# Optimization experiments

Hardware: AMD Instinct MI355X
Metric: run time of the kernel (lower is better)

## Reference

```python
import jax, jax.numpy as jnp
import numpy as np

# DCRNN (PEMS-BAY scale) constants
N = 325      # num_nodes
B = 64       # batch_size
T = 12       # encoder seq_len
HZ = 12      # decoder horizon
U = 64       # rnn_units
DIN = 2      # input_dim
DOUT = 1     # output_dim
K = 2        # max_diffusion_step
NM = K + 1   # num diffusion matrices (Chebyshev, single laplacian support)


def _glorot(key, shape):
    lim = float(np.sqrt(6.0 / (shape[0] + shape[1])))
    return jax.random.uniform(key, shape, jnp.float32, -lim, lim)


def setup_inputs() -> dict:
    key = jax.random.key(0)
    ks = jax.random.split(key, 8)
    # random symmetric adjacency -> scaled Laplacian support (lambda_max ~= 2 approx)
    a = np.asarray(jax.random.uniform(ks[0], (N, N)))
    a = (a + a.T) * 0.5
    a = a * (a > 0.9)
    d = a.sum(1)
    dinv = 1.0 / np.sqrt(np.maximum(d, 1e-8))
    L = np.eye(N, dtype=np.float32) - (dinv[:, None] * a * dinv[None, :]).astype(np.float32)
    support = jnp.asarray(L - np.eye(N, dtype=np.float32))  # 2L/lambda_max - I with lambda_max=2

    def cell_params(k, din):
        f = (din + U) * NM
        k1, k2 = jax.random.split(k)
        return dict(gate_W=_glorot(k1, (f, 2 * U)), gate_b=jnp.zeros((2 * U,), jnp.float32),
                    cand_W=_glorot(k2, (f, U)), cand_b=jnp.zeros((U,), jnp.float32))

    inp = {"inputs": jax.random.normal(ks[1], (T, B, N * DIN), jnp.float32),
           "support": support}
    for name, din, kk in [("enc0", DIN, ks[2]), ("enc1", U, ks[3]),
                          ("dec0", DOUT, ks[4]), ("dec1", U, ks[5])]:
        for pn, v in cell_params(kk, din).items():
            inp[f"{name}_{pn}"] = v
    inp["proj_W"] = _glorot(ks[6], (U, DOUT))
    inp["proj_b"] = jnp.zeros((DOUT,), jnp.float32)
    return inp


def _gconv(x, support, W, b):
    # x: (B, N, F). Chebyshev diffusion: x0=x, x1=Lx, x2=2Lx1-x0, ...
    xs = [x]
    x0, x1 = x, jnp.einsum('mn,bnf->bmf', support, x)
    xs.append(x1)
    for _ in range(2, K + 1):
        x2 = 2.0 * jnp.einsum('mn,bnf->bmf', support, x1) - x0
        xs.append(x2)
        x0, x1 = x1, x2
    xk = jnp.concatenate(xs, axis=-1)  # (B, N, NM*F)
    return xk @ W + b


def _gru_cell(x, h, support, gW, gb, cW, cb):
    # diffusion-conv GRU: r,u gates then candidate
    ru = jax.nn.sigmoid(_gconv(jnp.concatenate([x, h], -1), support, gW, gb))
    r, u = jnp.split(ru, 2, axis=-1)
    c = jnp.tanh(_gconv(jnp.concatenate([x, r * h], -1), support, cW, cb))
    return u * h + (1.0 - u) * c


def reference(inputs, support,
              enc0_gate_W, enc0_gate_b, enc0_cand_W, enc0_cand_b,
              enc1_gate_W, enc1_gate_b, enc1_cand_W, enc1_cand_b,
              dec0_gate_W, dec0_gate_b, dec0_cand_W, dec0_cand_b,
              dec1_gate_W, dec1_gate_b, dec1_cand_W, dec1_cand_b,
              proj_W, proj_b):
    x_seq = inputs.reshape(T, B, N, DIN)
    h0 = jnp.zeros((B, N, U), inputs.dtype)

    def enc_step(carry, x):
        h_l0, h_l1 = carry
        h_l0 = _gru_cell(x, h_l0, support, enc0_gate_W, enc0_gate_b, enc0_cand_W, enc0_cand_b)
        h_l1 = _gru_cell(h_l0, h_l1, support, enc1_gate_W, enc1_gate_b, enc1_cand_W, enc1_cand_b)
        return (h_l0, h_l1), None

    (h_l0, h_l1), _ = jax.lax.scan(enc_step, (h0, h0), x_seq)

    def dec_step(carry, _):
        d_in, hd0, hd1 = carry
        hd0 = _gru_cell(d_in, hd0, support, dec0_gate_W, dec0_gate_b, dec0_cand_W, dec0_cand_b)
        hd1 = _gru_cell(hd0, hd1, support, dec1_gate_W, dec1_gate_b, dec1_cand_W, dec1_cand_b)
        out = hd1 @ proj_W + proj_b  # (B, N, DOUT)
        return (out, hd0, hd1), out.reshape(B, N * DOUT)

    start = jnp.zeros((B, N, DOUT), inputs.dtype)  # GO symbol
    _, outputs = jax.lax.scan(dec_step, (start, h_l0, h_l1), None, length=HZ)
    return outputs  # (horizon, B, N*DOUT)
```

## Files before the change

kernel.cpp:

```cpp
#include <hip/hip_runtime.h>

constexpr int N  = 325;
constexpr int B  = 64;
constexpr int T  = 12;
constexpr int HZ = 12;
constexpr int U  = 64;
constexpr int BN = B * N;

constexpr int SSTIL = 42;
constexpr int SSKC  = 11;
constexpr int XST   = 364;

typedef __attribute__((ext_vector_type(8))) short short8;
typedef __attribute__((ext_vector_type(4))) float floatx4;

__device__ inline unsigned short f2bf(float f) {
    unsigned u = __float_as_uint(f);
    u += 0x7fff + ((u >> 16) & 1);
    return (unsigned short)(u >> 16);
}
__device__ inline unsigned pack_hilo(float v) {
    const unsigned short hi = f2bf(v);
    const float hif = __uint_as_float(((unsigned)hi) << 16);
    const unsigned short lo = f2bf(v - hif);
    return (unsigned)hi | ((unsigned)lo << 16);
}
__device__ inline void unpack8(const uint4 u0, const uint4 u1,
                               short8& h, short8& l) {
    const unsigned uu[8] = {u0.x, u0.y, u0.z, u0.w, u1.x, u1.y, u1.z, u1.w};
    #pragma unroll
    for (int j = 0; j < 8; ++j) {
        h[j] = (short)(uu[j] & 0xffffu);
        l[j] = (short)(uu[j] >> 16);
    }
}


__global__ void zero_kernel(unsigned* __restrict__ p, long n) {
    long i = (long)blockIdx.x * blockDim.x + threadIdx.x;
    const long stride = (long)gridDim.x * blockDim.x;
    for (; i < n; i += stride) p[i] = 0u;
}

__global__ __launch_bounds__(256)
void s2_build(const float* __restrict__ S, float* __restrict__ S2)
{
    const int m = blockIdx.x;
    __shared__ float srow[N];
    for (int i = threadIdx.x; i < N; i += 256) srow[i] = S[m * N + i];
    __syncthreads();
    for (int c = threadIdx.x; c < N; c += 256) {
        float a = 0.f;
        for (int k = 0; k < N; ++k) a += srow[k] * S[k * N + c];
        S2[m * N + c] = a;
    }
}

__global__ __launch_bounds__(64)
void prepack_ss(const float* __restrict__ S, const float* __restrict__ S2,
                short* __restrict__ ssh, short* __restrict__ ssl)
{
    const int t = blockIdx.x, kc = blockIdx.y, lane = threadIdx.x;
    const int quad = lane >> 4, l15 = lane & 15;
    short8 hv, lv;
    #pragma unroll
    for (int j = 0; j < 8; ++j) {
        const int m = t * 16 + l15;
        const int k = kc * 32 + quad * 8 + j;
        float v = 0.f;
        if (k < N) {
            if (m < N) v = S[m * N + k];
            else if (m >= 336 && m < 336 + N) v = S2[(m - 336) * N + k];
        }
        const unsigned short hb = f2bf(v);
        hv[j] = (short)hb;
        lv[j] = (short)f2bf(v - __uint_as_float(((unsigned)hb) << 16));
    }
    const size_t off = ((size_t)(t * SSKC + kc) * 64 + lane);
    ((short8*)ssh)[off] = hv;
    ((short8*)ssl)[off] = lv;
}

__global__ __launch_bounds__(64)
void prepack_w(const float* __restrict__ W, short* __restrict__ Wh,
               short* __restrict__ Wl, int F, int Nout, int NT, int Z0KC)
{
    const int kc = blockIdx.x, n = blockIdx.y, lane = threadIdx.x;
    const int quad = lane >> 4, l15 = lane & 15;
    short8 hv, lv;
    #pragma unroll
    for (int j = 0; j < 8; ++j) {
        const int p   = kc * 32 + quad * 8 + j;
        const int col = n * 16 + l15;
        float w = 0.f;
        if (p < Z0KC * 32) {
            const int f = p;
            if (f < F)
                w = W[(size_t)f * Nout + col] - W[(size_t)(2 * F + f) * Nout + col];
        } else {
            const int q = p - Z0KC * 32;
            if (q < F)
                w = W[(size_t)(F + q) * Nout + col];
            else if (q < 2 * F)
                w = 2.f * W[(size_t)(2 * F + (q - F)) * Nout + col];
        }
        const unsigned short hb = f2bf(w);
        hv[j] = (short)hb;
        lv[j] = (short)f2bf(w - __uint_as_float(((unsigned)hb) << 16));
    }
    const size_t off = ((size_t)(kc * NT + n) * 64 + lane);
    ((short8*)Wh)[off] = hv;
    ((short8*)Wl)[off] = lv;
}

template<int DIN, int F, bool RM, bool ZV>
__device__ __forceinline__ void z0_frag(const float* __restrict__ x,
    const float* __restrict__ h, const float* __restrict__ ru,
    int row, int kc, int quad, short8& ah, short8& al)
{
    float v[8];
    if constexpr (ZV) {
        const int k0 = kc * 32 + quad * 8;
        if (k0 < 64) {
            const float4 a = *(const float4*)&x[(size_t)row * 64 + k0];
            const float4 b = *(const float4*)&x[(size_t)row * 64 + k0 + 4];
            v[0]=a.x; v[1]=a.y; v[2]=a.z; v[3]=a.w;
            v[4]=b.x; v[5]=b.y; v[6]=b.z; v[7]=b.w;
        } else {
            const int kk = k0 - 64;
            float4 a = *(const float4*)&h[(size_t)row * 64 + kk];
            float4 b = *(const float4*)&h[(size_t)row * 64 + kk + 4];
            if constexpr (RM) {
                const float4 ra = *(const float4*)&ru[(size_t)row * 128 + kk];
                const float4 rb = *(const float4*)&ru[(size_t)row * 128 + kk + 4];
                a.x *= ra.x; a.y *= ra.y; a.z *= ra.z; a.w *= ra.w;
                b.x *= rb.x; b.y *= rb.y; b.z *= rb.z; b.w *= rb.w;
            }
            v[0]=a.x; v[1]=a.y; v[2]=a.z; v[3]=a.w;
            v[4]=b.x; v[5]=b.y; v[6]=b.z; v[7]=b.w;
        }
    } else {
        #pragma unroll
        for (int j = 0; j < 8; ++j) {
            const int k = kc * 32 + quad * 8 + j;
            float t = 0.f;
            if (k < DIN) t = x[(size_t)row * DIN + k];
            else if (k < F) {
                t = h[(size_t)row * 64 + (k - DIN)];
                if constexpr (RM) t *= ru[(size_t)row * 128 + (k - DIN)];
            }
            v[j] = t;
        }
    }
    #pragma unroll
    for (int j = 0; j < 8; ++j) {
        const unsigned u = pack_hilo(v[j]);
        ah[j] = (short)(u & 0xffffu);
        al[j] = (short)(u >> 16);
    }
}

template<int DIN, int F, int YP, bool RMUL, bool VEC>
__device__ __forceinline__ void diffuse_body(
    const short8* __restrict__ ssh, const short8* __restrict__ ssl,
    const float* __restrict__ x, const float* __restrict__ h,
    const float* __restrict__ ru, unsigned* __restrict__ zcat,
    int cx, int b, unsigned* __restrict__ xls)
{
    const int c0 = cx * 32;
    const int tid = threadIdx.x, wave = tid >> 6, lane = tid & 63;
    const int quad = lane >> 4, l15 = lane & 15;

    if constexpr (VEC) {
        for (int idx4 = tid; idx4 < 352 * 8; idx4 += 896) {
            const int n = idx4 >> 3, f = (idx4 & 7) * 4, gf = c0 + f;
            uint4 pk = make_uint4(0u, 0u, 0u, 0u);
            if (n < N) {
                const int row = b * N + n;
                float4 v;
                if (gf < DIN) {
                    v = *(const float4*)&x[(size_t)row * DIN + gf];
                } else {
                    v = *(const float4*)&h[(size_t)row * U + (gf - DIN)];
                    if (RMUL) {
                        const float4 rv = *(const float4*)&ru[(size_t)row * 128 + (gf - DIN)];
                        v.x *= rv.x; v.y *= rv.y; v.z *= rv.z; v.w *= rv.w;
                    }
                }
                pk.x = pack_hilo(v.x); pk.y = pack_hilo(v.y);
                pk.z = pack_hilo(v.z); pk.w = pack_hilo(v.w);
            }
            xls[(f + 0) * XST + n] = pk.x;
            xls[(f + 1) * XST + n] = pk.y;
            xls[(f + 2) * XST + n] = pk.z;
            xls[(f + 3) * XST + n] = pk.w;
        }
    } else {
        for (int idx = tid; idx < 352 * 32; idx += 896) {
            const int n = idx >> 5, f = idx & 31, gf = c0 + f;
            unsigned u = 0u;
            if (n < N && gf < F) {
                const int row = b * N + n;
                float v;
                if (gf < DIN) {
                    v = x[(size_t)row * DIN + gf];
                } else {
                    v = h[(size_t)row * U + (gf - DIN)];
                    if (RMUL) v *= ru[(size_t)row * 128 + (gf - DIN)];
                }
                u = pack_hilo(v);
            }
            xls[f * XST + n] = u;
        }
    }
    __syncthreads();

    const int tb = wave * 3;

    floatx4 acc[3][2];
    #pragma unroll
    for (int i = 0; i < 3; ++i)
        #pragma unroll
        for (int n = 0; n < 2; ++n)
            acc[i][n] = (floatx4){0.f, 0.f, 0.f, 0.f};

    short8 cah[3], cal[3], nah[3], nal[3];
    #pragma unroll
    for (int i = 0; i < 3; ++i) {
        const size_t fo = (size_t)((tb + i) * SSKC) * 64 + lane;
        cah[i] = ssh[fo]; cal[i] = ssl[fo];
    }
    for (int kc = 0; kc < SSKC; ++kc) {
        if (kc + 1 < SSKC) {
            #pragma unroll
            for (int i = 0; i < 3; ++i) {
                const size_t fo = (size_t)((tb + i) * SSKC + kc + 1) * 64 + lane;
                nah[i] = ssh[fo]; nal[i] = ssl[fo];
            }
        }
        short8 bh[2], bl[2];
        const int koff = kc * 32 + quad * 8;
        #pragma unroll
        for (int n = 0; n < 2; ++n) {
            const uint4 u0 = *(const uint4*)&xls[(n * 16 + l15) * XST + koff];
            const uint4 u1 = *(const uint4*)&xls[(n * 16 + l15) * XST + koff + 4];
            unpack8(u0, u1, bh[n], bl[n]);
        }
        #pragma unroll
        for (int i = 0; i < 3; ++i)
            #pragma unroll
            for (int n = 0; n < 2; ++n) {
                acc[i][n] = __builtin_amdgcn_mfma_f32_16x16x32_bf16(cah[i], bh[n], acc[i][n], 0, 0, 0);
                acc[i][n] = __builtin_amdgcn_mfma_f32_16x16x32_bf16(cah[i], bl[n], acc[i][n], 0, 0, 0);
                acc[i][n] = __builtin_amdgcn_mfma_f32_16x16x32_bf16(cal[i], bh[n], acc[i][n], 0, 0, 0);
            }
        if (kc + 1 < SSKC) {
            #pragma unroll
            for (int i = 0; i < 3; ++i) { cah[i] = nah[i]; cal[i] = nal[i]; }
        }
    }

    #pragma unroll
    for (int i = 0; i < 3; ++i) {
        const int t = tb + i;
        #pragma unroll
        for (int n = 0; n < 2; ++n) {
            const int col = c0 + n * 16 + l15;
            if (col >= F) continue;
            #pragma unroll
            for (int r = 0; r < 4; ++r) {
                const int m = t * 16 + quad * 4 + r;
                if (m < N)
                    zcat[(size_t)(b * N + m) * YP + col] = pack_hilo(acc[i][n][r]);
                else if (m >= 336 && m < 336 + N)
                    zcat[(size_t)(b * N + (m - 336)) * YP + F + col] = pack_hilo(acc[i][n][r]);
            }
        }
    }
}


template<int DIN, int F, int Z0KC, int YKC, bool ZV>
__device__ __forceinline__ void gate_body(const unsigned* __restrict__ zcat,
    const float* __restrict__ x, const float* __restrict__ h,
    const short8* __restrict__ Wh, const short8* __restrict__ Wl,
    const float* __restrict__ bias, float* __restrict__ ruout, int bx, int nb)
{
    constexpr int YP = YKC * 32, NT = 4;
    const int tid = threadIdx.x, wave = tid >> 6, lane = tid & 63;
    const int quad = lane >> 4, l15 = lane & 15;
    const int row0 = bx * 64 + wave * 16;
    const int row = row0 + l15;

    floatx4 acc[NT];
    #pragma unroll
    for (int n = 0; n < NT; ++n) {
        const float bv = bias[(nb + n) * 16 + l15];
        acc[n] = (floatx4){bv, bv, bv, bv};
    }
    for (int kc = 0; kc < Z0KC; ++kc) {
        short8 ahi, alo;
        z0_frag<DIN, F, false, ZV>(x, h, nullptr, row, kc, quad, ahi, alo);
        const short8* __restrict__ wh = Wh + (size_t)(kc * 8 + nb) * 64 + lane;
        const short8* __restrict__ wl = Wl + (size_t)(kc * 8 + nb) * 64 + lane;
        #pragma unroll
        for (int n = 0; n < NT; ++n) {
            const short8 bh = wh[n * 64], bl = wl[n * 64];
            acc[n] = __builtin_amdgcn_mfma_f32_16x16x32_bf16(ahi, bh, acc[n], 0, 0, 0);
            acc[n] = __builtin_amdgcn_mfma_f32_16x16x32_bf16(ahi, bl, acc[n], 0, 0, 0);
            acc[n] = __builtin_amdgcn_mfma_f32_16x16x32_bf16(alo, bh, acc[n], 0, 0, 0);
        }
    }
    const unsigned* __restrict__ zrow = zcat + (size_t)row * YP + quad * 8;
    for (int kc = 0; kc < YKC; ++kc) {
        const uint4* p = (const uint4*)(zrow + kc * 32);
        short8 ahi, alo;
        unpack8(p[0], p[1], ahi, alo);
        const short8* __restrict__ wh = Wh + (size_t)((Z0KC + kc) * 8 + nb) * 64 + lane;
        const short8* __restrict__ wl = Wl + (size_t)((Z0KC + kc) * 8 + nb) * 64 + lane;
        #pragma unroll
        for (int n = 0; n < NT; ++n) {
            const short8 bh = wh[n * 64], bl = wl[n * 64];
            acc[n] = __builtin_amdgcn_mfma_f32_16x16x32_bf16(ahi, bh, acc[n], 0, 0, 0);
            acc[n] = __builtin_amdgcn_mfma_f32_16x16x32_bf16(ahi, bl, acc[n], 0, 0, 0);
            acc[n] = __builtin_amdgcn_mfma_f32_16x16x32_bf16(alo, bh, acc[n], 0, 0, 0);
        }
    }
    #pragma unroll
    for (int n = 0; n < NT; ++n) {
        const int col = (nb + n) * 16 + l15;
        #pragma unroll
        for (int r = 0; r < 4; ++r) {
            const int rw = row0 + quad * 4 + r;
            ruout[(size_t)rw * 128 + col] = 1.f / (1.f + __expf(-acc[n][r]));
        }
    }
}

template<int DIN, int F, int Z0KC, int YKC, bool ZV>
__device__ __forceinline__ void cand_body(const unsigned* __restrict__ zcat,
    const float* __restrict__ x, const float* __restrict__ h,
    const float* __restrict__ ru, const short8* __restrict__ Wh,
    const short8* __restrict__ Wl, const float* __restrict__ bias,
    float* __restrict__ hout, int bx, int nb)
{
    constexpr int YP = YKC * 32, NT = 2;
    const int tid = threadIdx.x, wave = tid >> 6, lane = tid & 63;
    const int quad = lane >> 4, l15 = lane & 15;
    const int row0 = bx * 64 + wave * 16;
    const int row = row0 + l15;

    floatx4 acc[NT];
    #pragma unroll
    for (int n = 0; n < NT; ++n) {
        const float bv = bias[(nb + n) * 16 + l15];
        acc[n] = (floatx4){bv, bv, bv, bv};
    }
    for (int kc = 0; kc < Z0KC; ++kc) {
        short8 ahi, alo;
        z0_frag<DIN, F, true, ZV>(x, h, ru, row, kc, quad, ahi, alo);
        const short8* __restrict__ wh = Wh + (size_t)(kc * 4 + nb) * 64 + lane;
        const short8* __restrict__ wl = Wl + (size_t)(kc * 4 + nb) * 64 + lane;
        #pragma unroll
        for (int n = 0; n < NT; ++n) {
            const short8 bh = wh[n * 64], bl = wl[n * 64];
            acc[n] = __builtin_amdgcn_mfma_f32_16x16x32_bf16(ahi, bh, acc[n], 0, 0, 0);
            acc[n] = __builtin_amdgcn_mfma_f32_16x16x32_bf16(ahi, bl, acc[n], 0, 0, 0);
            acc[n] = __builtin_amdgcn_mfma_f32_16x16x32_bf16(alo, bh, acc[n], 0, 0, 0);
        }
    }
    const unsigned* __restrict__ zrow = zcat + (size_t)row * YP + quad * 8;
    for (int kc = 0; kc < YKC; ++kc) {
        const uint4* p = (const uint4*)(zrow + kc * 32);
        short8 ahi, alo;
        unpack8(p[0], p[1], ahi, alo);
        const short8* __restrict__ wh = Wh + (size_t)((Z0KC + kc) * 4 + nb) * 64 + lane;
        const short8* __restrict__ wl = Wl + (size_t)((Z0KC + kc) * 4 + nb) * 64 + lane;
        #pragma unroll
        for (int n = 0; n < NT; ++n) {
            const short8 bh = wh[n * 64], bl = wl[n * 64];
            acc[n] = __builtin_amdgcn_mfma_f32_16x16x32_bf16(ahi, bh, acc[n], 0, 0, 0);
            acc[n] = __builtin_amdgcn_mfma_f32_16x16x32_bf16(ahi, bl, acc[n], 0, 0, 0);
            acc[n] = __builtin_amdgcn_mfma_f32_16x16x32_bf16(alo, bh, acc[n], 0, 0, 0);
        }
    }
    #pragma unroll
    for (int n = 0; n < NT; ++n) {
        const int col = (nb + n) * 16 + l15;
        #pragma unroll
        for (int r = 0; r < 4; ++r) {
            const int rw = row0 + quad * 4 + r;
            const float c  = tanhf(acc[n][r]);
            const float ug = ru[(size_t)rw * 128 + 64 + col];
            const float hv = h[(size_t)rw * 64 + col];
            hout[(size_t)rw * 64 + col] = ug * hv + (1.f - ug) * c;
        }
    }
}


template<int DIN, int F, int YP, bool RMUL, int CB, bool VEC>
__global__ __launch_bounds__(896, 7)
void diffuse_solo(const short8* __restrict__ ssh, const short8* __restrict__ ssl,
                  const float* __restrict__ x, const float* __restrict__ h,
                  const float* __restrict__ ru, unsigned* __restrict__ zcat)
{
    __shared__ __align__(16) unsigned xls[32 * XST];
    diffuse_body<DIN, F, YP, RMUL, VEC>(ssh, ssl, x, h, ru, zcat,
                                        CB + blockIdx.x, blockIdx.y, xls);
}

template<int DIN, int F, int Z0KC, int YKC, bool ZV>
__global__ __launch_bounds__(256)
void gate_cell(const unsigned* __restrict__ zcat, const float* __restrict__ x,
               const float* __restrict__ h, const short8* __restrict__ Wh,
               const short8* __restrict__ Wl, const float* __restrict__ bias,
               float* __restrict__ ru)
{
    gate_body<DIN, F, Z0KC, YKC, ZV>(zcat, x, h, Wh, Wl, bias, ru,
                                     blockIdx.x, blockIdx.y * 4);
}

template<int DIN, int F, int Z0KC, int YKC, bool ZV>
__global__ __launch_bounds__(256)
void cand_cell(const unsigned* __restrict__ zcat, const float* __restrict__ x,
               const float* __restrict__ h, const float* __restrict__ ru,
               const short8* __restrict__ Wh, const short8* __restrict__ Wl,
               const float* __restrict__ bias, float* __restrict__ hout)
{
    cand_body<DIN, F, Z0KC, YKC, ZV>(zcat, x, h, ru, Wh, Wl, bias, hout,
                                     blockIdx.x, blockIdx.y * 2);
}

__global__ __launch_bounds__(256)
void cand_proj(const unsigned* __restrict__ zcat, const float* __restrict__ x,
               const float* __restrict__ h, const float* __restrict__ ru,
               const short8* __restrict__ Wh, const short8* __restrict__ Wl,
               const float* __restrict__ bias, float* __restrict__ hout,
               const float* __restrict__ pW, const float* __restrict__ pb,
               float* __restrict__ outp, float* __restrict__ dec_in)
{
    constexpr int Z0KC = 4, YKC = 8, YP = 256, NT = 4;
    const int tid = threadIdx.x, wave = tid >> 6, lane = tid & 63;
    const int quad = lane >> 4, l15 = lane & 15;
    const int row0 = blockIdx.x * 64 + wave * 16;
    const int row = row0 + l15;

    floatx4 acc[NT];
    #pragma unroll
    for (int n = 0; n < NT; ++n) {
        const float bv = bias[n * 16 + l15];
        acc[n] = (floatx4){bv, bv, bv, bv};
    }
    for (int kc = 0; kc < Z0KC; ++kc) {
        short8 ahi, alo;
        z0_frag<64, 128, true, true>(x, h, ru, row, kc, quad, ahi, alo);
        const short8* __restrict__ wh = Wh + (size_t)(kc * 4) * 64 + lane;
        const short8* __restrict__ wl = Wl + (size_t)(kc * 4) * 64 + lane;
        #pragma unroll
        for (int n = 0; n < NT; ++n) {
            const short8 bh = wh[n * 64], bl = wl[n * 64];
            acc[n] = __builtin_amdgcn_mfma_f32_16x16x32_bf16(ahi, bh, acc[n], 0, 0, 0);
            acc[n] = __builtin_amdgcn_mfma_f32_16x16x32_bf16(ahi, bl, acc[n], 0, 0, 0);
            acc[n] = __builtin_amdgcn_mfma_f32_16x16x32_bf16(alo, bh, acc[n], 0, 0, 0);
        }
    }
    const unsigned* __restrict__ zrow = zcat + (size_t)row * YP + quad * 8;
    for (int kc = 0; kc < YKC; ++kc) {
        const uint4* p = (const uint4*)(zrow + kc * 32);
        short8 ahi, alo;
        unpack8(p[0], p[1], ahi, alo);
        const short8* __restrict__ wh = Wh + (size_t)((Z0KC + kc) * 4) * 64 + lane;
        const short8* __restrict__ wl = Wl + (size_t)((Z0KC + kc) * 4) * 64 + lane;
        #pragma unroll
        for (int n = 0; n < NT; ++n) {
            const short8 bh = wh[n * 64], bl = wl[n * 64];
            acc[n] = __builtin_amdgcn_mfma_f32_16x16x32_bf16(ahi, bh, acc[n], 0, 0, 0);
            acc[n] = __builtin_amdgcn_mfma_f32_16x16x32_bf16(ahi, bl, acc[n], 0, 0, 0);
            acc[n] = __builtin_amdgcn_mfma_f32_16x16x32_bf16(alo, bh, acc[n], 0, 0, 0);
        }
    }
    float pr[4] = {0.f, 0.f, 0.f, 0.f};
    #pragma unroll
    for (int n = 0; n < NT; ++n) {
        const int col = n * 16 + l15;
        const float pw = pW[col];
        #pragma unroll
        for (int r = 0; r < 4; ++r) {
            const int rw = row0 + quad * 4 + r;
            const float c  = tanhf(acc[n][r]);
            const float ug = ru[(size_t)rw * 128 + 64 + col];
            const float hv = h[(size_t)rw * 64 + col];
            const float hn = ug * hv + (1.f - ug) * c;
            hout[(size_t)rw * 64 + col] = hn;
            pr[r] += hn * pw;
        }
    }
    #pragma unroll
    for (int r = 0; r < 4; ++r) {
        float v = pr[r];
        v += __shfl_xor(v, 1); v += __shfl_xor(v, 2);
        v += __shfl_xor(v, 4); v += __shfl_xor(v, 8);
        if (l15 == 0) {
            const int rw = row0 + quad * 4 + r;
            const float o = v + pb[0];
            outp[rw]   = o;
            dec_in[rw] = o;
        }
    }
}


struct DuoDP {
    const short8 *ssh, *ssl;
    const float *xA, *hA, *ruA; unsigned* zA;
    const float *xB, *hB, *ruB; unsigned* zB;
    int cA, cbB;
};

template<bool RM>
__global__ __launch_bounds__(896, 7)
void diffuse_duo(DuoDP P)
{
    __shared__ __align__(16) unsigned xls[32 * XST];
    if ((int)blockIdx.x < P.cA)
        diffuse_body<2, 66, 160, RM, false>(P.ssh, P.ssl, P.xA, P.hA, P.ruA,
                                            P.zA, blockIdx.x, blockIdx.y, xls);
    else
        diffuse_body<64, 128, 256, RM, true>(P.ssh, P.ssl, P.xB, P.hB, P.ruB,
                                             P.zB, P.cbB + blockIdx.x - P.cA,
                                             blockIdx.y, xls);
}

struct DuoGP {
    const unsigned* zA; const float *xA, *hA;
    const short8 *WhA, *WlA; const float* bA; float* ruA;
    const unsigned* zB; const float *xB, *hB;
    const short8 *WhB, *WlB; const float* bB; float* ruB;
};

__global__ __launch_bounds__(256)
void gate_duo(DuoGP P)
{
    if (blockIdx.z == 0)
        gate_body<2, 66, 3, 5, false>(P.zA, P.xA, P.hA, P.WhA, P.WlA, P.bA,
                                      P.ruA, blockIdx.x, blockIdx.y * 4);
    else
        gate_body<64, 128, 4, 8, true>(P.zB, P.xB, P.hB, P.WhB, P.WlB, P.bB,
                                       P.ruB, blockIdx.x, blockIdx.y * 4);
}

struct DuoCP {
    const unsigned* zA; const float *xA, *hA, *ruA;
    const short8 *WhA, *WlA; const float* bA; float* hoA;
    const unsigned* zB; const float *xB, *hB, *ruB;
    const short8 *WhB, *WlB; const float* bB; float* hoB;
};

__global__ __launch_bounds__(256)
void cand_duo(DuoCP P)
{
    if (blockIdx.z == 0)
        cand_body<2, 66, 3, 5, false>(P.zA, P.xA, P.hA, P.ruA, P.WhA, P.WlA,
                                      P.bA, P.hoA, blockIdx.x, blockIdx.y * 2);
    else
        cand_body<64, 128, 4, 8, true>(P.zB, P.xB, P.hB, P.ruB, P.WhB, P.WlB,
                                       P.bB, P.hoB, blockIdx.x, blockIdx.y * 2);
}


extern "C" void kernel_launch(void* const* d_in, const int* in_sizes, int n_in,
                              void* d_out, int out_size, void* d_ws, size_t ws_size,
                              hipStream_t stream)
{
    const float* inputs = (const float*)d_in[0];
    const float* S      = (const float*)d_in[1];
    const float* Wt[4][4];
    for (int l = 0; l < 4; ++l)
        for (int j = 0; j < 4; ++j)
            Wt[l][j] = (const float*)d_in[2 + l * 4 + j];
    const float* pW = (const float*)d_in[18];
    const float* pb = (const float*)d_in[19];
    float* out = (float*)d_out;

    float*    ws     = (float*)d_ws;
    float*    H0[2]  = {ws, ws + (size_t)BN * U};
    float*    H1[2]  = {ws + 2 * (size_t)BN * U, ws + 3 * (size_t)BN * U};
    float*    dec_in = ws + 4 * (size_t)BN * U;
    float*    ruA    = dec_in + BN;
    float*    ruB    = ruA + (size_t)BN * 128;
    unsigned* zcatA  = (unsigned*)(ruB + (size_t)BN * 128);
    unsigned* zcatB  = zcatA + (size_t)BN * 160;
    float*    S2     = (float*)(zcatB + (size_t)BN * 256);
    char*     pp     = (char*)(S2 + (size_t)N * N);
    pp = (char*)(((uintptr_t)pp + 15) & ~(uintptr_t)15);

    short* ssh = (short*)pp;
    short* ssl = ssh + (size_t)SSTIL * SSKC * 64 * 8;
    char*  wpbase = (char*)(ssl + (size_t)SSTIL * SSKC * 64 * 8);

    const int Fs[4]   = {66, 128, 65, 128};
    const int KPs[4]  = {256, 384, 256, 384};
    const int Z0s[4]  = {3, 4, 3, 4};
    short *Wgh[4], *Wgl[4], *Wch[4], *Wcl[4];
    size_t off = 0;
    for (int l = 0; l < 4; ++l) {
        const size_t ge = (size_t)KPs[l] * 128, ce = (size_t)KPs[l] * 64;
        Wgh[l] = (short*)(wpbase + off); off += ge * 2;
        Wgl[l] = (short*)(wpbase + off); off += ge * 2;
        Wch[l] = (short*)(wpbase + off); off += ce * 2;
        Wcl[l] = (short*)(wpbase + off); off += ce * 2;
    }

    const long zn = (long)BN * (4 * U) + BN + (long)BN * 256 + (long)BN * (160 + 256);
    zero_kernel<<<2048, 256, 0, stream>>>((unsigned*)ws, zn);

    s2_build<<<N, 256, 0, stream>>>(S, S2);
    prepack_ss<<<dim3(SSTIL, SSKC), 64, 0, stream>>>(S, S2, ssh, ssl);
    for (int l = 0; l < 4; ++l) {
        prepack_w<<<dim3(KPs[l] / 32, 8), 64, 0, stream>>>(Wt[l][0], Wgh[l], Wgl[l],
                                                           Fs[l], 128, 8, Z0s[l]);
        prepack_w<<<dim3(KPs[l] / 32, 4), 64, 0, stream>>>(Wt[l][2], Wch[l], Wcl[l],
                                                           Fs[l], 64, 4, Z0s[l]);
    }

    const short8* SSH = (const short8*)ssh;
    const short8* SSL = (const short8*)ssl;
    int p0 = 0, p1 = 0;

    for (int s = 0; s <= T; ++s) {
        const float* x0 = inputs + (size_t)s * BN * 2;
        const bool a = (s < T), b1 = (s >= 1);
        if (a && b1) {
            DuoDP dp{SSH, SSL, x0, H0[p0], nullptr, zcatA,
                     H0[p0], H1[p1], nullptr, zcatB, 3, 0};
            diffuse_duo<false><<<dim3(7, B), 896, 0, stream>>>(dp);
            DuoGP gp{zcatA, x0, H0[p0], (short8*)Wgh[0], (short8*)Wgl[0], Wt[0][1], ruA,
                     zcatB, H0[p0], H1[p1], (short8*)Wgh[1], (short8*)Wgl[1], Wt[1][1], ruB};
            gate_duo<<<dim3(BN / 64, 2, 2), 256, 0, stream>>>(gp);
            DuoDP dp2{SSH, SSL, x0, H0[p0], ruA, zcatA,
                      H0[p0], H1[p1], ruB, zcatB, 3, 2};
            diffuse_duo<true><<<dim3(5, B), 896, 0, stream>>>(dp2);
            DuoCP cp{zcatA, x0, H0[p0], ruA, (short8*)Wch[0], (short8*)Wcl[0], Wt[0][3], H0[p0 ^ 1],
                     zcatB, H0[p0], H1[p1], ruB, (short8*)Wch[1], (short8*)Wcl[1], Wt[1][3], H1[p1 ^ 1]};
            cand_duo<<<dim3(BN / 64, 2, 2), 256, 0, stream>>>(cp);
            p0 ^= 1; p1 ^= 1;
        } else if (a) {
            diffuse_solo<2, 66, 160, false, 0, false><<<dim3(3, B), 896, 0, stream>>>(
                SSH, SSL, x0, H0[p0], nullptr, zcatA);
            gate_cell<2, 66, 3, 5, false><<<dim3(BN / 64, 2), 256, 0, stream>>>(
                zcatA, x0, H0[p0], (short8*)Wgh[0], (short8*)Wgl[0], Wt[0][1], ruA);
            diffuse_solo<2, 66, 160, true, 0, false><<<dim3(3, B), 896, 0, stream>>>(
                SSH, SSL, x0, H0[p0], ruA, zcatA);
            cand_cell<2, 66, 3, 5, false><<<dim3(BN / 64, 2), 256, 0, stream>>>(
                zcatA, x0, H0[p0], ruA, (short8*)Wch[0], (short8*)Wcl[0], Wt[0][3], H0[p0 ^ 1]);
            p0 ^= 1;
        } else {
            diffuse_solo<64, 128, 256, false, 0, true><<<dim3(4, B), 896, 0, stream>>>(
                SSH, SSL, H0[p0], H1[p1], nullptr, zcatB);
            gate_cell<64, 128, 4, 8, true><<<dim3(BN / 64, 2), 256, 0, stream>>>(
                zcatB, H0[p0], H1[p1], (short8*)Wgh[1], (short8*)Wgl[1], Wt[1][1], ruB);
            diffuse_solo<64, 128, 256, true, 2, true><<<dim3(2, B), 896, 0, stream>>>(
                SSH, SSL, H0[p0], H1[p1], ruB, zcatB);
            cand_cell<64, 128, 4, 8, true><<<dim3(BN / 64, 2), 256, 0, stream>>>(
                zcatB, H0[p0], H1[p1], ruB, (short8*)Wch[1], (short8*)Wcl[1], Wt[1][3], H1[p1 ^ 1]);
            p1 ^= 1;
        }
    }

    for (int hz = 0; hz < HZ; ++hz) {
        diffuse_solo<1, 65, 160, false, 0, false><<<dim3(3, B), 896, 0, stream>>>(
            SSH, SSL, dec_in, H0[p0], nullptr, zcatB);
        gate_cell<1, 65, 3, 5, false><<<dim3(BN / 64, 2), 256, 0, stream>>>(
            zcatB, dec_in, H0[p0], (short8*)Wgh[2], (short8*)Wgl[2], Wt[2][1], ruA);
        diffuse_solo<1, 65, 160, true, 0, false><<<dim3(3, B), 896, 0, stream>>>(
            SSH, SSL, dec_in, H0[p0], ruA, zcatB);
        cand_cell<1, 65, 3, 5, false><<<dim3(BN / 64, 2), 256, 0, stream>>>(
            zcatB, dec_in, H0[p0], ruA, (short8*)Wch[2], (short8*)Wcl[2], Wt[2][3], H0[p0 ^ 1]);
        p0 ^= 1;
        diffuse_solo<64, 128, 256, false, 0, true><<<dim3(4, B), 896, 0, stream>>>(
            SSH, SSL, H0[p0], H1[p1], nullptr, zcatB);
        gate_cell<64, 128, 4, 8, true><<<dim3(BN / 64, 2), 256, 0, stream>>>(
            zcatB, H0[p0], H1[p1], (short8*)Wgh[3], (short8*)Wgl[3], Wt[3][1], ruA);
        diffuse_solo<64, 128, 256, true, 2, true><<<dim3(2, B), 896, 0, stream>>>(
            SSH, SSL, H0[p0], H1[p1], ruA, zcatB);
        cand_proj<<<BN / 64, 256, 0, stream>>>(
            zcatB, H0[p0], H1[p1], ruA, (short8*)Wch[3], (short8*)Wcl[3], Wt[3][3],
            H1[p1 ^ 1], pW, pb, out + (size_t)hz * BN, dec_in);
        p1 ^= 1;
    }
}
```

Before: 3.964 ms.

## Fuse gate, reset-diffusion and candidate phases into one per-batch tail kernel

Replaces the gate kernel, the second diffusion launch and the candidate kernel with a single tail kernel that uses one 896-thread block per batch element. The block computes the r/u gates, then runs the r-scaled diffusion chunks and the candidate GEMM with __syncthreads between phases. This cuts three launches per GRU cell down to one and keeps intermediate data block-local. The cost is far fewer blocks in flight (64 or 128 instead of hundreds), so per-step parallelism and occupancy drop, and each block serially runs diffusion chunks that were previously spread across the grid.

New measurement: 13.98 ms. 3.53x slower.

```diff
diff --git a/kernel.cpp b/kernel.cpp
--- a/kernel.cpp
+++ b/kernel.cpp
@@ -281,121 +281,203 @@
 
 
 template<int DIN, int F, int Z0KC, int YKC, bool ZV>
-__device__ __forceinline__ void gate_body(const unsigned* __restrict__ zcat,
+__device__ __forceinline__ void g_phase(const unsigned* __restrict__ zcat,
     const float* __restrict__ x, const float* __restrict__ h,
     const short8* __restrict__ Wh, const short8* __restrict__ Wl,
-    const float* __restrict__ bias, float* __restrict__ ruout, int bx, int nb)
-{
-    constexpr int YP = YKC * 32, NT = 4;
+    const float* __restrict__ bias, float* __restrict__ ruout, int b)
+{
+    constexpr int YP = YKC * 32;
     const int tid = threadIdx.x, wave = tid >> 6, lane = tid & 63;
     const int quad = lane >> 4, l15 = lane & 15;
-    const int row0 = bx * 64 + wave * 16;
-    const int row = row0 + l15;
-
-    floatx4 acc[NT];
-    #pragma unroll
-    for (int n = 0; n < NT; ++n) {
-        const float bv = bias[(nb + n) * 16 + l15];
-        acc[n] = (floatx4){bv, bv, bv, bv};
-    }
-    for (int kc = 0; kc < Z0KC; ++kc) {
-        short8 ahi, alo;
-        z0_frag<DIN, F, false, ZV>(x, h, nullptr, row, kc, quad, ahi, alo);
-        const short8* __restrict__ wh = Wh + (size_t)(kc * 8 + nb) * 64 + lane;
-        const short8* __restrict__ wl = Wl + (size_t)(kc * 8 + nb) * 64 + lane;
-        #pragma unroll
-        for (int n = 0; n < NT; ++n) {
-            const short8 bh = wh[n * 64], bl = wl[n * 64];
-            acc[n] = __builtin_amdgcn_mfma_f32_16x16x32_bf16(ahi, bh, acc[n], 0, 0, 0);
-            acc[n] = __builtin_amdgcn_mfma_f32_16x16x32_bf16(ahi, bl, acc[n], 0, 0, 0);
-            acc[n] = __builtin_amdgcn_mfma_f32_16x16x32_bf16(alo, bh, acc[n], 0, 0, 0);
-        }
-    }
-    const unsigned* __restrict__ zrow = zcat + (size_t)row * YP + quad * 8;
-    for (int kc = 0; kc < YKC; ++kc) {
-        const uint4* p = (const uint4*)(zrow + kc * 32);
-        short8 ahi, alo;
-        unpack8(p[0], p[1], ahi, alo);
-        const short8* __restrict__ wh = Wh + (size_t)((Z0KC + kc) * 8 + nb) * 64 + lane;
-        const short8* __restrict__ wl = Wl + (size_t)((Z0KC + kc) * 8 + nb) * 64 + lane;
-        #pragma unroll
-        for (int n = 0; n < NT; ++n) {
-            const short8 bh = wh[n * 64], bl = wl[n * 64];
-            acc[n] = __builtin_amdgcn_mfma_f32_16x16x32_bf16(ahi, bh, acc[n], 0, 0, 0);
-            acc[n] = __builtin_amdgcn_mfma_f32_16x16x32_bf16(ahi, bl, acc[n], 0, 0, 0);
-            acc[n] = __builtin_amdgcn_mfma_f32_16x16x32_bf16(alo, bh, acc[n], 0, 0, 0);
-        }
-    }
-    #pragma unroll
-    for (int n = 0; n < NT; ++n) {
-        const int col = (nb + n) * 16 + l15;
-        #pragma unroll
-        for (int r = 0; r < 4; ++r) {
-            const int rw = row0 + quad * 4 + r;
-            ruout[(size_t)rw * 128 + col] = 1.f / (1.f + __expf(-acc[n][r]));
-        }
-    }
-}
-
-template<int DIN, int F, int Z0KC, int YKC, bool ZV>
-__device__ __forceinline__ void cand_body(const unsigned* __restrict__ zcat,
-    const float* __restrict__ x, const float* __restrict__ h,
+
+    for (int bt = wave; bt < 21; bt += 14) {
+        const int row0 = bt * 16;
+        const int rr = min(row0 + l15, N - 1);
+        const int grow = b * N + rr;
+        floatx4 acc[8];
+        #pragma unroll
+        for (int n = 0; n < 8; ++n) {
+            const float bv = bias[n * 16 + l15];
+            acc[n] = (floatx4){bv, bv, bv, bv};
+        }
+        for (int kc = 0; kc < Z0KC; ++kc) {
+            short8 ahi, alo;
+            z0_frag<DIN, F, false, ZV>(x, h, nullptr, grow, kc, quad, ahi, alo);
+            const short8* __restrict__ wh = Wh + (size_t)(kc * 8) * 64 + lane;
+            const short8* __restrict__ wl = Wl + (size_t)(kc * 8) * 64 + lane;
+            #pragma unroll
+            for (int n = 0; n < 8; ++n) {
+                const short8 bh = wh[n * 64], bl = wl[n * 64];
+                acc[n] = __builtin_amdgcn_mfma_f32_16x16x32_bf16(ahi, bh, acc[n], 0, 0, 0);
+                acc[n] = __builtin_amdgcn_mfma_f32_16x16x32_bf16(ahi, bl, acc[n], 0, 0, 0);
+                acc[n] = __builtin_amdgcn_mfma_f32_16x16x32_bf16(alo, bh, acc[n], 0, 0, 0);
+            }
+        }
+        const unsigned* __restrict__ zrow = zcat + (size_t)grow * YP + quad * 8;
+        for (int kc = 0; kc < YKC; ++kc) {
+            const uint4* p = (const uint4*)(zrow + kc * 32);
+            short8 ahi, alo;
+            unpack8(p[0], p[1], ahi, alo);
+            const short8* __restrict__ wh = Wh + (size_t)((Z0KC + kc) * 8) * 64 + lane;
+            const short8* __restrict__ wl = Wl + (size_t)((Z0KC + kc) * 8) * 64 + lane;
+            #pragma unroll
+            for (int n = 0; n < 8; ++n) {
+                const short8 bh = wh[n * 64], bl = wl[n * 64];
+                acc[n] = __builtin_amdgcn_mfma_f32_16x16x32_bf16(ahi, bh, acc[n], 0, 0, 0);
+                acc[n] = __builtin_amdgcn_mfma_f32_16x16x32_bf16(ahi, bl, acc[n], 0, 0, 0);
+                acc[n] = __builtin_amdgcn_mfma_f32_16x16x32_bf16(alo, bh, acc[n], 0, 0, 0);
+            }
+        }
+        #pragma unroll
+        for (int n = 0; n < 8; ++n) {
+            const int col = n * 16 + l15;
+            #pragma unroll
+            for (int r = 0; r < 4; ++r) {
+                const int row = row0 + quad * 4 + r;
+                if (row < N)
+                    ruout[((size_t)b * N + row) * 128 + col] =
+                        1.f / (1.f + __expf(-acc[n][r]));
+            }
+        }
+    }
+}
+
+template<int DIN, int F, int Z0KC, int YKC, bool ZV, bool PROJ>
+__device__ __forceinline__ void c_phase(const unsigned* __restrict__ zcat,
+    const float* __restrict__ x, const float* __restrict__ hin,
     const float* __restrict__ ru, const short8* __restrict__ Wh,
     const short8* __restrict__ Wl, const float* __restrict__ bias,
-    float* __restrict__ hout, int bx, int nb)
-{
-    constexpr int YP = YKC * 32, NT = 2;
+    float* __restrict__ hout, int b, const float* __restrict__ pW,
+    const float* __restrict__ pb, float* __restrict__ outp,
+    float* __restrict__ dec_in)
+{
+    constexpr int YP = YKC * 32;
     const int tid = threadIdx.x, wave = tid >> 6, lane = tid & 63;
     const int quad = lane >> 4, l15 = lane & 15;
-    const int row0 = bx * 64 + wave * 16;
-    const int row = row0 + l15;
-
-    floatx4 acc[NT];
-    #pragma unroll
-    for (int n = 0; n < NT; ++n) {
-        const float bv = bias[(nb + n) * 16 + l15];
-        acc[n] = (floatx4){bv, bv, bv, bv};
-    }
-    for (int kc = 0; kc < Z0KC; ++kc) {
-        short8 ahi, alo;
-        z0_frag<DIN, F, true, ZV>(x, h, ru, row, kc, quad, ahi, alo);
-        const short8* __restrict__ wh = Wh + (size_t)(kc * 4 + nb) * 64 + lane;
-        const short8* __restrict__ wl = Wl + (size_t)(kc * 4 + nb) * 64 + lane;
-        #pragma unroll
-        for (int n = 0; n < NT; ++n) {
-            const short8 bh = wh[n * 64], bl = wl[n * 64];
-            acc[n] = __builtin_amdgcn_mfma_f32_16x16x32_bf16(ahi, bh, acc[n], 0, 0, 0);
-            acc[n] = __builtin_amdgcn_mfma_f32_16x16x32_bf16(ahi, bl, acc[n], 0, 0, 0);
-            acc[n] = __builtin_amdgcn_mfma_f32_16x16x32_bf16(alo, bh, acc[n], 0, 0, 0);
-        }
-    }
-    const unsigned* __restrict__ zrow = zcat + (size_t)row * YP + quad * 8;
-    for (int kc = 0; kc < YKC; ++kc) {
-        const uint4* p = (const uint4*)(zrow + kc * 32);
-        short8 ahi, alo;
-        unpack8(p[0], p[1], ahi, alo);
-        const short8* __restrict__ wh = Wh + (size_t)((Z0KC + kc) * 4 + nb) * 64 + lane;
-        const short8* __restrict__ wl = Wl + (size_t)((Z0KC + kc) * 4 + nb) * 64 + lane;
-        #pragma unroll
-        for (int n = 0; n < NT; ++n) {
-            const short8 bh = wh[n * 64], bl = wl[n * 64];
-            acc[n] = __builtin_amdgcn_mfma_f32_16x16x32_bf16(ahi, bh, acc[n], 0, 0, 0);
-            acc[n] = __builtin_amdgcn_mfma_f32_16x16x32_bf16(ahi, bl, acc[n], 0, 0, 0);
-            acc[n] = __builtin_amdgcn_mfma_f32_16x16x32_bf16(alo, bh, acc[n], 0, 0, 0);
-        }
-    }
-    #pragma unroll
-    for (int n = 0; n < NT; ++n) {
-        const int col = (nb + n) * 16 + l15;
-        #pragma unroll
-        for (int r = 0; r < 4; ++r) {
-            const int rw = row0 + quad * 4 + r;
-            const float c  = tanhf(acc[n][r]);
-            const float ug = ru[(size_t)rw * 128 + 64 + col];
-            const float hv = h[(size_t)rw * 64 + col];
-            hout[(size_t)rw * 64 + col] = ug * hv + (1.f - ug) * c;
-        }
-    }
+
+    for (int bt = wave; bt < 21; bt += 14) {
+        const int row0 = bt * 16;
+        const int rr = min(row0 + l15, N - 1);
+        const int grow = b * N + rr;
+        floatx4 acc[4];
+        #pragma unroll
+        for (int n = 0; n < 4; ++n) {
+            const float bv = bias[n * 16 + l15];
+            acc[n] = (floatx4){bv, bv, bv, bv};
+        }
+        for (int kc = 0; kc < Z0KC; ++kc) {
+            short8 ahi, alo;
+            z0_frag<DIN, F, true, ZV>(x, hin, ru, grow, kc, quad, ahi, alo);
+            const short8* __restrict__ wh = Wh + (size_t)(kc * 4) * 64 + lane;
+            const short8* __restrict__ wl = Wl + (size_t)(kc * 4) * 64 + lane;
+            #pragma unroll
+            for (int n = 0; n < 4; ++n) {
+                const short8 bh = wh[n * 64], bl = wl[n * 64];
+                acc[n] = __builtin_amdgcn_mfma_f32_16x16x32_bf16(ahi, bh, acc[n], 0, 0, 0);
+                acc[n] = __builtin_amdgcn_mfma_f32_16x16x32_bf16(ahi, bl, acc[n], 0, 0, 0);
+                acc[n] = __builtin_amdgcn_mfma_f32_16x16x32_bf16(alo, bh, acc[n], 0, 0, 0);
+            }
+        }
+        const unsigned* __restrict__ zrow = zcat + (size_t)grow * YP + quad * 8;
+        for (int kc = 0; kc < YKC; ++kc) {
+            const uint4* p = (const uint4*)(zrow + kc * 32);
+            short8 ahi, alo;
+            unpack8(p[0], p[1], ahi, alo);
+            const short8* __restrict__ wh = Wh + (size_t)((Z0KC + kc) * 4) * 64 + lane;
+            const short8* __restrict__ wl = Wl + (size_t)((Z0KC + kc) * 4) * 64 + lane;
+            #pragma unroll
+            for (int n = 0; n < 4; ++n) {
+                const short8 bh = wh[n * 64], bl = wl[n * 64];
+                acc[n] = __builtin_amdgcn_mfma_f32_16x16x32_bf16(ahi, bh, acc[n], 0, 0, 0);
+                acc[n] = __builtin_amdgcn_mfma_f32_16x16x32_bf16(ahi, bl, acc[n], 0, 0, 0);
+                acc[n] = __builtin_amdgcn_mfma_f32_16x16x32_bf16(alo, bh, acc[n], 0, 0, 0);
+            }
+        }
+        float pr[4] = {0.f, 0.f, 0.f, 0.f};
+        #pragma unroll
+        for (int n = 0; n < 4; ++n) {
+            const int col = n * 16 + l15;
+            float pw = 0.f;
+            if constexpr (PROJ) pw = pW[col];
+            #pragma unroll
+            for (int r = 0; r < 4; ++r) {
+                const int row = row0 + quad * 4 + r;
+                if (row < N) {
+                    const size_t g2 = (size_t)b * N + row;
+                    const float c  = tanhf(acc[n][r]);
+                    const float ug = ru[g2 * 128 + 64 + col];
+                    const float hv = hin[g2 * 64 + col];
+                    const float hn = ug * hv + (1.f - ug) * c;
+                    hout[g2 * 64 + col] = hn;
+                    if constexpr (PROJ) pr[r] += hn * pw;
+                }
+            }
+        }
+        if constexpr (PROJ) {
+            #pragma unroll
+            for (int r = 0; r < 4; ++r) {
+                float v = pr[r];
+                v += __shfl_xor(v, 1); v += __shfl_xor(v, 2);
+                v += __shfl_xor(v, 4); v += __shfl_xor(v, 8);
+                if (l15 == 0) {
+                    const int row = row0 + quad * 4 + r;
+                    if (row < N) {
+                        const float o = v + pb[0];
+                        outp[b * N + row]   = o;
+                        dec_in[b * N + row] = o;
+                    }
+                }
+            }
+        }
+    }
+}
+
+
+struct TailP {
+    unsigned* zcat;
+    const float *x, *hin; float* hout;
+    float* ru;
+    const short8 *Wgh, *Wgl, *Wch, *Wcl;
+    const float *gb, *cb;
+    const short8 *ssh, *ssl;
+};
+
+template<int DIN, int F, int NCH, int CB2, int Z0KC, int YKC, bool ZV, bool PROJ>
+__device__ __forceinline__ void tail_body(const TailP& P, int b,
+    unsigned* __restrict__ xls, const float* pW, const float* pb,
+    float* outp, float* dec_in)
+{
+    g_phase<DIN, F, Z0KC, YKC, ZV>(P.zcat, P.x, P.hin, P.Wgh, P.Wgl, P.gb, P.ru, b);
+    for (int cx = CB2; cx < NCH; ++cx) {
+        __syncthreads();
+        diffuse_body<DIN, F, YKC * 32, true, ZV>(P.ssh, P.ssl, P.x, P.hin, P.ru,
+                                                 P.zcat, cx, b, xls);
+    }
+    __syncthreads();
+    c_phase<DIN, F, Z0KC, YKC, ZV, PROJ>(P.zcat, P.x, P.hin, P.ru, P.Wch, P.Wcl,
+                                         P.cb, P.hout, b, pW, pb, outp, dec_in);
+}
+
+template<int DIN, int F, int NCH, int CB2, int Z0KC, int YKC, bool ZV, bool PROJ>
+__global__ __launch_bounds__(896, 4)
+void tail_cell(TailP P, const float* pW, const float* pb,
+               float* outp, float* dec_in)
+{
+    __shared__ __align__(16) unsigned xls[32 * XST];
+    tail_body<DIN, F, NCH, CB2, Z0KC, YKC, ZV, PROJ>(P, blockIdx.y, xls,
+                                                     pW, pb, outp, dec_in);
+}
+
+__global__ __launch_bounds__(896, 4)
+void tail_duo(TailP A, TailP B)
+{
+    __shared__ __align__(16) unsigned xls[32 * XST];
+    if (blockIdx.x == 0)
+        tail_body<2, 66, 3, 0, 3, 5, false, false>(A, blockIdx.y, xls,
+                                                   nullptr, nullptr, nullptr, nullptr);
+    else
+        tail_body<64, 128, 4, 2, 4, 8, true, false>(B, blockIdx.y, xls,
+                                                    nullptr, nullptr, nullptr, nullptr);
 }
 
 
@@ -410,162 +492,24 @@
                                         CB + blockIdx.x, blockIdx.y, xls);
 }
 
-template<int DIN, int F, int Z0KC, int YKC, bool ZV>
-__global__ __launch_bounds__(256)
-void gate_cell(const unsigned* __restrict__ zcat, const float* __restrict__ x,
-               const float* __restrict__ h, const short8* __restrict__ Wh,
-               const short8* __restrict__ Wl, const float* __restrict__ bias,
-               float* __restrict__ ru)
-{
-    gate_body<DIN, F, Z0KC, YKC, ZV>(zcat, x, h, Wh, Wl, bias, ru,
-                                     blockIdx.x, blockIdx.y * 4);
-}
-
-template<int DIN, int F, int Z0KC, int YKC, bool ZV>
-__global__ __launch_bounds__(256)
-void cand_cell(const unsigned* __restrict__ zcat, const float* __restrict__ x,
-               const float* __restrict__ h, const float* __restrict__ ru,
-               const short8* __restrict__ Wh, const short8* __restrict__ Wl,
-               const float* __restrict__ bias, float* __restrict__ hout)
-{
-    cand_body<DIN, F, Z0KC, YKC, ZV>(zcat, x, h, ru, Wh, Wl, bias, hout,
-                                     blockIdx.x, blockIdx.y * 2);
-}
-
-__global__ __launch_bounds__(256)
-void cand_proj(const unsigned* __restrict__ zcat, const float* __restrict__ x,
-               const float* __restrict__ h, const float* __restrict__ ru,
-               const short8* __restrict__ Wh, const short8* __restrict__ Wl,
-               const float* __restrict__ bias, float* __restrict__ hout,
-               const float* __restrict__ pW, const float* __restrict__ pb,
-               float* __restrict__ outp, float* __restrict__ dec_in)
-{
-    constexpr int Z0KC = 4, YKC = 8, YP = 256, NT = 4;
-    const int tid = threadIdx.x, wave = tid >> 6, lane = tid & 63;
-    const int quad = lane >> 4, l15 = lane & 15;
-    const int row0 = blockIdx.x * 64 + wave * 16;
-    const int row = row0 + l15;
-
-    floatx4 acc[NT];
-    #pragma unroll
-    for (int n = 0; n < NT; ++n) {
-        const float bv = bias[n * 16 + l15];
-        acc[n] = (floatx4){bv, bv, bv, bv};
-    }
-    for (int kc = 0; kc < Z0KC; ++kc) {
-        short8 ahi, alo;
-        z0_frag<64, 128, true, true>(x, h, ru, row, kc, quad, ahi, alo);
-        const short8* __restrict__ wh = Wh + (size_t)(kc * 4) * 64 + lane;
-        const short8* __restrict__ wl = Wl + (size_t)(kc * 4) * 64 + lane;
-        #pragma unroll
-        for (int n = 0; n < NT; ++n) {
-            const short8 bh = wh[n * 64], bl = wl[n * 64];
-            acc[n] = __builtin_amdgcn_mfma_f32_16x16x32_bf16(ahi, bh, acc[n], 0, 0, 0);
-            acc[n] = __builtin_amdgcn_mfma_f32_16x16x32_bf16(ahi, bl, acc[n], 0, 0, 0);
-            acc[n] = __builtin_amdgcn_mfma_f32_16x16x32_bf16(alo, bh, acc[n], 0, 0, 0);
-        }
-    }
-    const unsigned* __restrict__ zrow = zcat + (size_t)row * YP + quad * 8;
-    for (int kc = 0; kc < YKC; ++kc) {
-        const uint4* p = (const uint4*)(zrow + kc * 32);
-        short8 ahi, alo;
-        unpack8(p[0], p[1], ahi, alo);
-        const short8* __restrict__ wh = Wh + (size_t)((Z0KC + kc) * 4) * 64 + lane;
-        const short8* __restrict__ wl = Wl + (size_t)((Z0KC + kc) * 4) * 64 + lane;
-        #pragma unroll
-        for (int n = 0; n < NT; ++n) {
-            const short8 bh = wh[n * 64], bl = wl[n * 64];
-            acc[n] = __builtin_amdgcn_mfma_f32_16x16x32_bf16(ahi, bh, acc[n], 0, 0, 0);
-            acc[n] = __builtin_amdgcn_mfma_f32_16x16x32_bf16(ahi, bl, acc[n], 0, 0, 0);
-            acc[n] = __builtin_amdgcn_mfma_f32_16x16x32_bf16(alo, bh, acc[n], 0, 0, 0);
-        }
-    }
-    float pr[4] = {0.f, 0.f, 0.f, 0.f};
-    #pragma unroll
-    for (int n = 0; n < NT; ++n) {
-        const int col = n * 16 + l15;
-        const float pw = pW[col];
-        #pragma unroll
-        for (int r = 0; r < 4; ++r) {
-            const int rw = row0 + quad * 4 + r;
-            const float c  = tanhf(acc[n][r]);
-            const float ug = ru[(size_t)rw * 128 + 64 + col];
-            const float hv = h[(size_t)rw * 64 + col];
-            const float hn = ug * hv + (1.f - ug) * c;
-            hout[(size_t)rw * 64 + col] = hn;
-            pr[r] += hn * pw;
-        }
-    }
-    #pragma unroll
-    for (int r = 0; r < 4; ++r) {
-        float v = pr[r];
-        v += __shfl_xor(v, 1); v += __shfl_xor(v, 2);
-        v += __shfl_xor(v, 4); v += __shfl_xor(v, 8);
-        if (l15 == 0) {
-            const int rw = row0 + quad * 4 + r;
-            const float o = v + pb[0];
-            outp[rw]   = o;
-            dec_in[rw] = o;
-        }
-    }
-}
-
-
 struct DuoDP {
     const short8 *ssh, *ssl;
-    const float *xA, *hA, *ruA; unsigned* zA;
-    const float *xB, *hB, *ruB; unsigned* zB;
-    int cA, cbB;
+    const float *xA, *hA; unsigned* zA;
+    const float *xB, *hB; unsigned* zB;
+    int cA;
 };
 
-template<bool RM>
 __global__ __launch_bounds__(896, 7)
 void diffuse_duo(DuoDP P)
 {
     __shared__ __align__(16) unsigned xls[32 * XST];
     if ((int)blockIdx.x < P.cA)
-        diffuse_body<2, 66, 160, RM, false>(P.ssh, P.ssl, P.xA, P.hA, P.ruA,
-                                            P.zA, blockIdx.x, blockIdx.y, xls);
+        diffuse_body<2, 66, 160, false, false>(P.ssh, P.ssl, P.xA, P.hA, nullptr,
+                                               P.zA, blockIdx.x, blockIdx.y, xls);
     else
-        diffuse_body<64, 128, 256, RM, true>(P.ssh, P.ssl, P.xB, P.hB, P.ruB,
-                                             P.zB, P.cbB + blockIdx.x - P.cA,
-                                             blockIdx.y, xls);
-}
-
-struct DuoGP {
-    const unsigned* zA; const float *xA, *hA;
-    const short8 *WhA, *WlA; const float* bA; float* ruA;
-    const unsigned* zB; const float *xB, *hB;
-    const short8 *WhB, *WlB; const float* bB; float* ruB;
-};
-
-__global__ __launch_bounds__(256)
-void gate_duo(DuoGP P)
-{
-    if (blockIdx.z == 0)
-        gate_body<2, 66, 3, 5, false>(P.zA, P.xA, P.hA, P.WhA, P.WlA, P.bA,
-                                      P.ruA, blockIdx.x, blockIdx.y * 4);
-    else
-        gate_body<64, 128, 4, 8, true>(P.zB, P.xB, P.hB, P.WhB, P.WlB, P.bB,
-                                       P.ruB, blockIdx.x, blockIdx.y * 4);
-}
-
-struct DuoCP {
-    const unsigned* zA; const float *xA, *hA, *ruA;
-    const short8 *WhA, *WlA; const float* bA; float* hoA;
-    const unsigned* zB; const float *xB, *hB, *ruB;
-    const short8 *WhB, *WlB; const float* bB; float* hoB;
-};
-
-__global__ __launch_bounds__(256)
-void cand_duo(DuoCP P)
-{
-    if (blockIdx.z == 0)
-        cand_body<2, 66, 3, 5, false>(P.zA, P.xA, P.hA, P.ruA, P.WhA, P.WlA,
-                                      P.bA, P.hoA, blockIdx.x, blockIdx.y * 2);
-    else
-        cand_body<64, 128, 4, 8, true>(P.zB, P.xB, P.hB, P.ruB, P.WhB, P.WlB,
-                                       P.bB, P.hoB, blockIdx.x, blockIdx.y * 2);
+        diffuse_body<64, 128, 256, false, true>(P.ssh, P.ssl, P.xB, P.hB, nullptr,
+                                                P.zB, blockIdx.x - P.cA,
+                                                blockIdx.y, xls);
 }
 
 
@@ -628,42 +572,40 @@
     const short8* SSL = (const short8*)ssl;
     int p0 = 0, p1 = 0;
 
+    auto mkTail = [&](unsigned* z, const float* x, float* hin, float* hout,
+                      float* ru, int l) {
+        TailP t;
+        t.zcat = z; t.x = x; t.hin = hin; t.hout = hout; t.ru = ru;
+        t.Wgh = (const short8*)Wgh[l]; t.Wgl = (const short8*)Wgl[l];
+        t.Wch = (const short8*)Wch[l]; t.Wcl = (const short8*)Wcl[l];
+        t.gb = Wt[l][1]; t.cb = Wt[l][3];
+        t.ssh = SSH; t.ssl = SSL;
+        return t;
+    };
+
     for (int s = 0; s <= T; ++s) {
         const float* x0 = inputs + (size_t)s * BN * 2;
         const bool a = (s < T), b1 = (s >= 1);
         if (a && b1) {
-            DuoDP dp{SSH, SSL, x0, H0[p0], nullptr, zcatA,
-                     H0[p0], H1[p1], nullptr, zcatB, 3, 0};
-            diffuse_duo<false><<<dim3(7, B), 896, 0, stream>>>(dp);
-            DuoGP gp{zcatA, x0, H0[p0], (short8*)Wgh[0], (short8*)Wgl[0], Wt[0][1], ruA,
-                     zcatB, H0[p0], H1[p1], (short8*)Wgh[1], (short8*)Wgl[1], Wt[1][1], ruB};
-            gate_duo<<<dim3(BN / 64, 2, 2), 256, 0, stream>>>(gp);
-            DuoDP dp2{SSH, SSL, x0, H0[p0], ruA, zcatA,
-                      H0[p0], H1[p1], ruB, zcatB, 3, 2};
-            diffuse_duo<true><<<dim3(5, B), 896, 0, stream>>>(dp2);
-            DuoCP cp{zcatA, x0, H0[p0], ruA, (short8*)Wch[0], (short8*)Wcl[0], Wt[0][3], H0[p0 ^ 1],
-                     zcatB, H0[p0], H1[p1], ruB, (short8*)Wch[1], (short8*)Wcl[1], Wt[1][3], H1[p1 ^ 1]};
-            cand_duo<<<dim3(BN / 64, 2, 2), 256, 0, stream>>>(cp);
+            DuoDP dp{SSH, SSL, x0, H0[p0], zcatA, H0[p0], H1[p1], zcatB, 3};
+            diffuse_duo<<<dim3(7, B), 896, 0, stream>>>(dp);
+            tail_duo<<<dim3(2, B), 896, 0, stream>>>(
+                mkTail(zcatA, x0, H0[p0], H0[p0 ^ 1], ruA, 0),
+                mkTail(zcatB, H0[p0], H1[p1], H1[p1 ^ 1], ruB, 1));
             p0 ^= 1; p1 ^= 1;
         } else if (a) {
             diffuse_solo<2, 66, 160, false, 0, false><<<dim3(3, B), 896, 0, stream>>>(
                 SSH, SSL, x0, H0[p0], nullptr, zcatA);
-            gate_cell<2, 66, 3, 5, false><<<dim3(BN / 64, 2), 256, 0, stream>>>(
-                zcatA, x0, H0[p0], (short8*)Wgh[0], (short8*)Wgl[0], Wt[0][1], ruA);
-            diffuse_solo<2, 66, 160, true, 0, false><<<dim3(3, B), 896, 0, stream>>>(
-                SSH, SSL, x0, H0[p0], ruA, zcatA);
-            cand_cell<2, 66, 3, 5, false><<<dim3(BN / 64, 2), 256, 0, stream>>>(
-                zcatA, x0, H0[p0], ruA, (short8*)Wch[0], (short8*)Wcl[0], Wt[0][3], H0[p0 ^ 1]);
+            tail_cell<2, 66, 3, 0, 3, 5, false, false><<<dim3(1, B), 896, 0, stream>>>(
+                mkTail(zcatA, x0, H0[p0], H0[p0 ^ 1], ruA, 0),
+                nullptr, nullptr, nullptr, nullptr);
             p0 ^= 1;
         } else {
             diffuse_solo<64, 128, 256, false, 0, true><<<dim3(4, B), 896, 0, stream>>>(
                 SSH, SSL, H0[p0], H1[p1], nullptr, zcatB);
-            gate_cell<64, 128, 4, 8, true><<<dim3(BN / 64, 2), 256, 0, stream>>>(
-                zcatB, H0[p0], H1[p1], (short8*)Wgh[1], (short8*)Wgl[1], Wt[1][1], ruB);
-            diffuse_solo<64, 128, 256, true, 2, true><<<dim3(2, B), 896, 0, stream>>>(
-                SSH, SSL, H0[p0], H1[p1], ruB, zcatB);
-            cand_cell<64, 128, 4, 8, true><<<dim3(BN / 64, 2), 256, 0, stream>>>(
-                zcatB, H0[p0], H1[p1], ruB, (short8*)Wch[1], (short8*)Wcl[1], Wt[1][3], H1[p1 ^ 1]);
+            tail_cell<64, 128, 4, 2, 4, 8, true, false><<<dim3(1, B), 896, 0, stream>>>(
+                mkTail(zcatB, H0[p0], H1[p1], H1[p1 ^ 1], ruB, 1),
+                nullptr, nullptr, nullptr, nullptr);
             p1 ^= 1;
         }
     }
@@ -671,22 +613,15 @@
     for (int hz = 0; hz < HZ; ++hz) {
         diffuse_solo<1, 65, 160, false, 0, false><<<dim3(3, B), 896, 0, stream>>>(
             SSH, SSL, dec_in, H0[p0], nullptr, zcatB);
-        gate_cell<1, 65, 3, 5, false><<<dim3(BN / 64, 2), 256, 0, stream>>>(
-            zcatB, dec_in, H0[p0], (short8*)Wgh[2], (short8*)Wgl[2], Wt[2][1], ruA);
-        diffuse_solo<1, 65, 160, true, 0, false><<<dim3(3, B), 896, 0, stream>>>(
-            SSH, SSL, dec_in, H0[p0], ruA, zcatB);
-        cand_cell<1, 65, 3, 5, false><<<dim3(BN / 64, 2), 256, 0, stream>>>(
-            zcatB, dec_in, H0[p0], ruA, (short8*)Wch[2], (short8*)Wcl[2], Wt[2][3], H0[p0 ^ 1]);
+        tail_cell<1, 65, 3, 0, 3, 5, false, false><<<dim3(1, B), 896, 0, stream>>>(
+            mkTail(zcatB, dec_in, H0[p0], H0[p0 ^ 1], ruA, 2),
+            nullptr, nullptr, nullptr, nullptr);
         p0 ^= 1;
         diffuse_solo<64, 128, 256, false, 0, true><<<dim3(4, B), 896, 0, stream>>>(
             SSH, SSL, H0[p0], H1[p1], nullptr, zcatB);
-        gate_cell<64, 128, 4, 8, true><<<dim3(BN / 64, 2), 256, 0, stream>>>(
-            zcatB, H0[p0], H1[p1], (short8*)Wgh[3], (short8*)Wgl[3], Wt[3][1], ruA);
-        diffuse_solo<64, 128, 256, true, 2, true><<<dim3(2, B), 896, 0, stream>>>(
-            SSH, SSL, H0[p0], H1[p1], ruA, zcatB);
-        cand_proj<<<BN / 64, 256, 0, stream>>>(
-            zcatB, H0[p0], H1[p1], ruA, (short8*)Wch[3], (short8*)Wcl[3], Wt[3][3],
-            H1[p1 ^ 1], pW, pb, out + (size_t)hz * BN, dec_in);
+        tail_cell<64, 128, 4, 2, 4, 8, true, true><<<dim3(1, B), 896, 0, stream>>>(
+            mkTail(zcatB, H0[p0], H1[p1], H1[p1 ^ 1], ruA, 3),
+            pW, pb, out + (size_t)hz * BN, dec_in);
         p1 ^= 1;
     }
 }
```
